# Optimization experiments

Measured on AMD Instinct MI355X. Metric: run time of the kernel, lower is better.

Reference implementation:

```python
import jax, jax.numpy as jnp
import numpy as np

N = 50000          # nodes
E_RAND = 800000    # random edges (avg degree 16)
IN, HID, HEADS, OUT = 256, 64, 4, 40
NEG_SLOPE = 0.2    # PyG GATConv default leaky_relu slope
BN_EPS = 1e-5


def setup_inputs() -> dict:
    key = jax.random.key(0)
    ks = jax.random.split(key, 24)
    x = jax.random.normal(ks[0], (N, IN), jnp.float32)
    ei = jax.random.randint(ks[1], (2, E_RAND), 0, N)
    loops = jnp.arange(N, dtype=ei.dtype)
    edge_index = jnp.concatenate([ei, jnp.stack([loops, loops])], axis=1)  # add self loops (PyG default)
    s = 0.1
    d = {
        "x": x,
        "edge_index": edge_index,
        "W0": jax.random.normal(ks[2], (IN, HEADS * HID), jnp.float32) * s,
        "a_src0": jax.random.normal(ks[3], (HEADS, HID), jnp.float32) * s,
        "a_dst0": jax.random.normal(ks[4], (HEADS, HID), jnp.float32) * s,
        "b0": jax.random.normal(ks[5], (HEADS * HID,), jnp.float32) * s,
        "bn0_g": jnp.ones((HEADS * HID,), jnp.float32),
        "bn0_b": jnp.zeros((HEADS * HID,), jnp.float32),
        "bn0_m": jax.random.normal(ks[6], (HEADS * HID,), jnp.float32) * s,
        "bn0_v": jax.random.uniform(ks[7], (HEADS * HID,), jnp.float32, 0.5, 1.5),
        "W1": jax.random.normal(ks[8], (HEADS * HID, HEADS * HID), jnp.float32) * s,
        "a_src1": jax.random.normal(ks[9], (HEADS, HID), jnp.float32) * s,
        "a_dst1": jax.random.normal(ks[10], (HEADS, HID), jnp.float32) * s,
        "b1": jax.random.normal(ks[11], (HEADS * HID,), jnp.float32) * s,
        "bn1_g": jnp.ones((HEADS * HID,), jnp.float32),
        "bn1_b": jnp.zeros((HEADS * HID,), jnp.float32),
        "bn1_m": jax.random.normal(ks[12], (HEADS * HID,), jnp.float32) * s,
        "bn1_v": jax.random.uniform(ks[13], (HEADS * HID,), jnp.float32, 0.5, 1.5),
        "W2": jax.random.normal(ks[14], (HEADS * HID, OUT), jnp.float32) * s,
        "a_src2": jax.random.normal(ks[15], (1, OUT), jnp.float32) * s,
        "a_dst2": jax.random.normal(ks[16], (1, OUT), jnp.float32) * s,
        "b2": jax.random.normal(ks[17], (OUT,), jnp.float32) * s,
    }
    return d


def gat_conv(x, edge_index, W, att_src, att_dst, heads, ch):
    """PyG GATConv (eval mode): gather -> leaky_relu attn -> segment softmax -> scatter add."""
    src, dst = edge_index[0], edge_index[1]
    h = (x @ W).reshape(-1, heads, ch)                       # [N,H,C]
    a_s = jnp.einsum('nhc,hc->nh', h, att_src)
    a_d = jnp.einsum('nhc,hc->nh', h, att_dst)
    e = jax.nn.leaky_relu(a_s[src] + a_d[dst], NEG_SLOPE)    # [E,H]
    m = jax.ops.segment_max(e, dst, num_segments=N)
    m = jax.lax.stop_gradient(jnp.where(jnp.isfinite(m), m, 0.0))
    p = jnp.exp(e - m[dst])
    denom = jax.ops.segment_sum(p, dst, num_segments=N)
    alpha = p / (denom[dst] + 1e-16)                         # [E,H]
    msg = h[src] * alpha[:, :, None]                         # [E,H,C]
    return jax.ops.segment_sum(msg, dst, num_segments=N)     # [N,H,C]


def _bn(h, g, b, m, v):
    return g * (h - m) * jax.lax.rsqrt(v + BN_EPS) + b


def reference(x, edge_index, W0, a_src0, a_dst0, b0, bn0_g, bn0_b, bn0_m, bn0_v,
              W1, a_src1, a_dst1, b1, bn1_g, bn1_b, bn1_m, bn1_v,
              W2, a_src2, a_dst2, b2):
    h = gat_conv(x, edge_index, W0, a_src0, a_dst0, HEADS, HID).reshape(N, HEADS * HID) + b0
    h = jax.nn.elu(_bn(h, bn0_g, bn0_b, bn0_m, bn0_v))
    h = gat_conv(h, edge_index, W1, a_src1, a_dst1, HEADS, HID).reshape(N, HEADS * HID) + b1
    h = jax.nn.elu(_bn(h, bn1_g, bn1_b, bn1_m, bn1_v))
    out = gat_conv(h, edge_index, W2, a_src2, a_dst2, 1, OUT).reshape(N, OUT) + b2
    return out
```

## Files before the change

kernel.cpp:

```cpp
#include <hip/hip_runtime.h>
#include <cstdint>
#include <cstddef>

constexpr int kN = 50000;
constexpr float kSlope = 0.2f;
constexpr float kBnEps = 1e-5f;

static inline int ceil_div(int a, int b) { return (a + b - 1) / b; }

typedef __attribute__((ext_vector_type(8))) _Float16 half8;
typedef __attribute__((ext_vector_type(8))) unsigned short ushortx8;
typedef __attribute__((ext_vector_type(4))) float f32x4;

__device__ inline unsigned short f2h_us(float f) {
  _Float16 h = (_Float16)f;
  return *(unsigned short*)&h;
}


__global__ void k_degree(const int* __restrict__ dst, int* __restrict__ deg, int E) {
  int e = blockIdx.x * blockDim.x + threadIdx.x;
  if (e < E) atomicAdd(&deg[dst[e]], 1);
}

__global__ void k_scan1(const int* __restrict__ deg, int* __restrict__ rp,
                        int* __restrict__ bsum, int n) {
  __shared__ int sm[256];
  int i = blockIdx.x * 256 + threadIdx.x;
  int v = (i < n) ? deg[i] : 0;
  sm[threadIdx.x] = v;
  __syncthreads();
  for (int off = 1; off < 256; off <<= 1) {
    int t = (threadIdx.x >= off) ? sm[threadIdx.x - off] : 0;
    __syncthreads();
    sm[threadIdx.x] += t;
    __syncthreads();
  }
  if (i < n) rp[i + 1] = sm[threadIdx.x];
  if (threadIdx.x == 255) bsum[blockIdx.x] = sm[255];
}

__global__ void k_scan2(int* bsum, int nb) {
  __shared__ int sm[256];
  int v = (threadIdx.x < nb) ? bsum[threadIdx.x] : 0;
  sm[threadIdx.x] = v;
  __syncthreads();
  for (int off = 1; off < 256; off <<= 1) {
    int t = (threadIdx.x >= off) ? sm[threadIdx.x - off] : 0;
    __syncthreads();
    sm[threadIdx.x] += t;
    __syncthreads();
  }
  if (threadIdx.x < nb) bsum[threadIdx.x] = sm[threadIdx.x] - v;
}

__global__ void k_scan3(int* __restrict__ rp, const int* __restrict__ bsum, int n) {
  int i = blockIdx.x * 256 + threadIdx.x;
  if (i < n) rp[i + 1] += bsum[blockIdx.x];
  if (i == 0) rp[0] = 0;
}

__global__ void k_scatter(const int* __restrict__ src, const int* __restrict__ dst,
                          const int* __restrict__ rp, int* __restrict__ cur,
                          int* __restrict__ csr, int E) {
  int e = blockIdx.x * blockDim.x + threadIdx.x;
  if (e < E) {
    int d = dst[e];
    int pos = rp[d] + atomicAdd(&cur[d], 1);
    csr[pos] = src[e];
  }
}


__global__ void k_cast(const float* __restrict__ in, unsigned short* __restrict__ out, int n4) {
  int i = blockIdx.x * blockDim.x + threadIdx.x;
  if (i >= n4) return;
  float4 v = ((const float4*)in)[i];
  ushort4 o;
  o.x = f2h_us(v.x);
  o.y = f2h_us(v.y);
  o.z = f2h_us(v.z);
  o.w = f2h_us(v.w);
  ((ushort4*)out)[i] = o;
}

__global__ void k_transW3(const float* __restrict__ W0, unsigned short* __restrict__ Wt0,
                          const float* __restrict__ W1, unsigned short* __restrict__ Wt1,
                          const float* __restrict__ W2, unsigned short* __restrict__ Wt2) {
  int i = blockIdx.x * blockDim.x + threadIdx.x;
  const int S0 = 256 * 256, S1 = 256 * 256, S2 = 128 * 256;
  if (i < S0) {
    int nc = i >> 8, k = i & 255;
    Wt0[i] = f2h_us(W0[(size_t)k * 256 + nc]);
  } else if (i < S0 + S1) {
    int j = i - S0;
    int nc = j >> 8, k = j & 255;
    Wt1[j] = f2h_us(W1[(size_t)k * 256 + nc]);
  } else if (i < S0 + S1 + S2) {
    int j = i - S0 - S1;
    int nc = j >> 8, k = j & 255;
    Wt2[j] = (nc < 40) ? f2h_us(W2[(size_t)k * 40 + nc]) : (unsigned short)0;
  }
}


__global__ __launch_bounds__(256) void k_mfma_gemm(
    const unsigned short* __restrict__ A, const unsigned short* __restrict__ Bt,
    unsigned short* __restrict__ C, const float* __restrict__ asrc,
    const float* __restrict__ adst, float* __restrict__ a_s, float* __restrict__ a_d, int M,
    int K, int Nc, int ldc, int heads, int acols) {
  constexpr int BM = 128, BK = 32, LDR = 40;
  __shared__ unsigned short As[BM * LDR];
  __shared__ unsigned short Bs[BM * LDR];
  int tid = threadIdx.x;
  int wave = tid >> 6, lane = tid & 63;
  int quad = lane >> 4, l16 = lane & 15;
  int wm = (wave & 1) * 64, wn = (wave >> 1) * 64;
  int bm = blockIdx.x * BM, bn = blockIdx.y * BM;
  f32x4 acc[4][4] = {};
  for (int k0 = 0; k0 < K; k0 += BK) {
#pragma unroll
    for (int it = 0; it < 2; it++) {
      int c = tid + it * 256;
      int row = c >> 2, part = c & 3;
      int gm = bm + row;
      ushortx8 va = (ushortx8)(0);
      if (gm < M) va = *(const ushortx8*)(A + (size_t)gm * K + k0 + part * 8);
      *(ushortx8*)(As + row * LDR + part * 8) = va;
      ushortx8 vb = *(const ushortx8*)(Bt + (size_t)(bn + row) * K + k0 + part * 8);
      *(ushortx8*)(Bs + row * LDR + part * 8) = vb;
    }
    __syncthreads();
    half8 af[4], bf[4];
#pragma unroll
    for (int i = 0; i < 4; i++) {
      af[i] = *(const half8*)(As + (wm + i * 16 + l16) * LDR + quad * 8);
      bf[i] = *(const half8*)(Bs + (wn + i * 16 + l16) * LDR + quad * 8);
    }
#pragma unroll
    for (int i = 0; i < 4; i++)
#pragma unroll
      for (int j = 0; j < 4; j++)
        acc[i][j] = __builtin_amdgcn_mfma_f32_16x16x32_f16(af[i], bf[j], acc[i][j], 0, 0, 0);
    __syncthreads();
  }
#pragma unroll
  for (int i = 0; i < 4; i++) {
#pragma unroll
    for (int j = 0; j < 4; j++) {
      int col = bn + wn + j * 16 + l16;
      if (col >= Nc) continue;
#pragma unroll
      for (int r = 0; r < 4; r++) {
        int row = bm + wm + i * 16 + quad * 4 + r;
        if (row < M) C[(size_t)row * ldc + col] = f2h_us(acc[i][j][r]);
      }
    }
  }
  int ghead = (bn + wn) >> 6;
  if (ghead < heads) {
    float asv[4], adv[4];
#pragma unroll
    for (int j = 0; j < 4; j++) {
      int col = bn + wn + j * 16 + l16;
      bool ok = col < acols;
      asv[j] = ok ? asrc[col] : 0.f;
      adv[j] = ok ? adst[col] : 0.f;
    }
#pragma unroll
    for (int i = 0; i < 4; i++) {
#pragma unroll
      for (int r = 0; r < 4; r++) {
        float s = acc[i][0][r] * asv[0] + acc[i][1][r] * asv[1] + acc[i][2][r] * asv[2] +
                  acc[i][3][r] * asv[3];
        float d = acc[i][0][r] * adv[0] + acc[i][1][r] * adv[1] + acc[i][2][r] * adv[2] +
                  acc[i][3][r] * adv[3];
#pragma unroll
        for (int mask = 1; mask <= 8; mask <<= 1) {
          s += __shfl_xor(s, mask, 64);
          d += __shfl_xor(d, mask, 64);
        }
        if (l16 == 0) {
          int row = bm + wm + i * 16 + quad * 4 + r;
          if (row < M) {
            a_s[row * heads + ghead] = s;
            a_d[row * heads + ghead] = d;
          }
        }
      }
    }
  }
}


__global__ __launch_bounds__(256) void k_attn_agg256(
    const int* __restrict__ rp, const int* __restrict__ csr, const _Float16* __restrict__ h,
    const float* __restrict__ a_s, const float* __restrict__ a_d, const float* __restrict__ bias,
    const float* __restrict__ bg, const float* __restrict__ bb, const float* __restrict__ bm,
    const float* __restrict__ bv, unsigned short* __restrict__ out, int n_nodes) {
  int wid = (blockIdx.x * blockDim.x + threadIdx.x) >> 6;
  int lane = threadIdx.x & 63;
  if (wid >= n_nodes) return;
  int n = wid;
  int beg = rp[n], end = rp[n + 1];
  int half = lane >> 5, l32 = lane & 31;
  int head = l32 >> 3;
  int c = l32 * 8;
  float ad = a_d[n * 4 + head];
  float acc[8] = {};
  float psum = 0.f;
  int e = beg;
  for (; e + 8 <= end; e += 8) {
    int s0 = csr[e + half];
    int s1 = csr[e + 2 + half];
    int s2 = csr[e + 4 + half];
    int s3 = csr[e + 6 + half];
    float x0 = a_s[s0 * 4 + head] + ad;
    float x1 = a_s[s1 * 4 + head] + ad;
    float x2 = a_s[s2 * 4 + head] + ad;
    float x3 = a_s[s3 * 4 + head] + ad;
    half8 v0 = *(const half8*)(h + (size_t)s0 * 256 + c);
    half8 v1 = *(const half8*)(h + (size_t)s1 * 256 + c);
    half8 v2 = *(const half8*)(h + (size_t)s2 * 256 + c);
    half8 v3 = *(const half8*)(h + (size_t)s3 * 256 + c);
    x0 = x0 > 0.f ? x0 : x0 * kSlope;
    x1 = x1 > 0.f ? x1 : x1 * kSlope;
    x2 = x2 > 0.f ? x2 : x2 * kSlope;
    x3 = x3 > 0.f ? x3 : x3 * kSlope;
    float p0 = __expf(x0), p1 = __expf(x1);
    float p2 = __expf(x2), p3 = __expf(x3);
    psum += (p0 + p1) + (p2 + p3);
#pragma unroll
    for (int j = 0; j < 8; j++) {
      acc[j] += (float)v0[j] * p0 + (float)v1[j] * p1;
      acc[j] += (float)v2[j] * p2 + (float)v3[j] * p3;
    }
  }
  for (; e + 2 <= end; e += 2) {
    int s0 = csr[e + half];
    float x0 = a_s[s0 * 4 + head] + ad;
    x0 = x0 > 0.f ? x0 : x0 * kSlope;
    float p0 = __expf(x0);
    psum += p0;
    half8 v0 = *(const half8*)(h + (size_t)s0 * 256 + c);
#pragma unroll
    for (int j = 0; j < 8; j++) acc[j] += (float)v0[j] * p0;
  }
  if (e < end && half == 0) {
    int s0 = csr[e];
    float x0 = a_s[s0 * 4 + head] + ad;
    x0 = x0 > 0.f ? x0 : x0 * kSlope;
    float p0 = __expf(x0);
    psum += p0;
    half8 v0 = *(const half8*)(h + (size_t)s0 * 256 + c);
#pragma unroll
    for (int j = 0; j < 8; j++) acc[j] += (float)v0[j] * p0;
  }
  psum += __shfl_xor(psum, 32, 64);
#pragma unroll
  for (int j = 0; j < 8; j++) acc[j] += __shfl_xor(acc[j], 32, 64);
  if (half == 0) {
    float rden = 1.f / (psum + 1e-16f);
    ushortx8 o;
#pragma unroll
    for (int j = 0; j < 8; j++) {
      float v = acc[j] * rden + bias[c + j];
      v = bg[c + j] * (v - bm[c + j]) * rsqrtf(bv[c + j] + kBnEps) + bb[c + j];
      v = v > 0.f ? v : (__expf(v) - 1.f);
      o[j] = f2h_us(v);
    }
    *(ushortx8*)(out + (size_t)n * 256 + c) = o;
  }
}


__global__ __launch_bounds__(256) void k_attn_agg40(
    const int* __restrict__ rp, const int* __restrict__ csr, const _Float16* __restrict__ h,
    const float* __restrict__ a_s, const float* __restrict__ a_d, const float* __restrict__ bias,
    float* __restrict__ out, int n_nodes) {
  int wid = (blockIdx.x * blockDim.x + threadIdx.x) >> 6;
  int lane = threadIdx.x & 63;
  if (wid >= n_nodes) return;
  int n = wid;
  int beg = rp[n], end = rp[n + 1];
  float ad = a_d[n];
  int grp = lane >> 3, l8 = lane & 7;
  int c = l8 * 8;
  float acc[8] = {};
  float psum = 0.f;
  for (int base = beg; base < end; base += 16) {
    int e0 = base + grp;
    int e1 = base + 8 + grp;
    if (e0 < end) {
      int s = csr[e0];
      float x = a_s[s] + ad;
      x = x > 0.f ? x : x * kSlope;
      float p = __expf(x);
      psum += p;
      half8 hv = *(const half8*)(h + (size_t)s * 64 + c);
#pragma unroll
      for (int j = 0; j < 8; j++) acc[j] += (float)hv[j] * p;
    }
    if (e1 < end) {
      int s = csr[e1];
      float x = a_s[s] + ad;
      x = x > 0.f ? x : x * kSlope;
      float p = __expf(x);
      psum += p;
      half8 hv = *(const half8*)(h + (size_t)s * 64 + c);
#pragma unroll
      for (int j = 0; j < 8; j++) acc[j] += (float)hv[j] * p;
    }
  }
#pragma unroll
  for (int mask = 8; mask <= 32; mask <<= 1) psum += __shfl_xor(psum, mask, 64);
#pragma unroll
  for (int j = 0; j < 8; j++) {
#pragma unroll
    for (int mask = 8; mask <= 32; mask <<= 1) acc[j] += __shfl_xor(acc[j], mask, 64);
  }
  if (lane < 5) {
    float rden = 1.f / (psum + 1e-16f);
    float4 o0, o1;
    o0.x = acc[0] * rden + bias[c + 0];
    o0.y = acc[1] * rden + bias[c + 1];
    o0.z = acc[2] * rden + bias[c + 2];
    o0.w = acc[3] * rden + bias[c + 3];
    o1.x = acc[4] * rden + bias[c + 4];
    o1.y = acc[5] * rden + bias[c + 5];
    o1.z = acc[6] * rden + bias[c + 6];
    o1.w = acc[7] * rden + bias[c + 7];
    *(float4*)(out + (size_t)n * 40 + c) = o0;
    *(float4*)(out + (size_t)n * 40 + c + 4) = o1;
  }
}


extern "C" void kernel_launch(void* const* d_in, const int* in_sizes, int n_in, void* d_out,
                              int out_size, void* d_ws, size_t ws_size, hipStream_t stream) {
  const float* x = (const float*)d_in[0];
  const int* ei = (const int*)d_in[1];
  const float* W0 = (const float*)d_in[2];
  const float* as0 = (const float*)d_in[3];
  const float* ad0 = (const float*)d_in[4];
  const float* b0 = (const float*)d_in[5];
  const float* bg0 = (const float*)d_in[6];
  const float* bb0 = (const float*)d_in[7];
  const float* bm0 = (const float*)d_in[8];
  const float* bv0 = (const float*)d_in[9];
  const float* W1 = (const float*)d_in[10];
  const float* as1 = (const float*)d_in[11];
  const float* ad1 = (const float*)d_in[12];
  const float* b1 = (const float*)d_in[13];
  const float* bg1 = (const float*)d_in[14];
  const float* bb1 = (const float*)d_in[15];
  const float* bm1 = (const float*)d_in[16];
  const float* bv1 = (const float*)d_in[17];
  const float* W2 = (const float*)d_in[18];
  const float* as2 = (const float*)d_in[19];
  const float* ad2 = (const float*)d_in[20];
  const float* b2 = (const float*)d_in[21];
  float* out = (float*)d_out;

  const int E = in_sizes[1] / 2;
  const int* srcIdx = ei;
  const int* dstIdx = ei + E;

  char* p = (char*)d_ws;
  auto alloc = [&](size_t bytes) -> void* {
    void* r = (void*)p;
    p += (bytes + 255) & ~(size_t)255;
    return r;
  };
  int* rp = (int*)alloc((kN + 1) * sizeof(int));
  int* degcur = (int*)alloc((size_t)2 * kN * sizeof(int));
  int* deg = degcur;
  int* cur = degcur + kN;
  int* bsum = (int*)alloc(256 * sizeof(int));
  int* csr = (int*)alloc((size_t)E * sizeof(int));
  float* a_s = (float*)alloc((size_t)kN * 4 * sizeof(float));
  float* a_d = (float*)alloc((size_t)kN * 4 * sizeof(float));
  unsigned short* x16 = (unsigned short*)alloc((size_t)kN * 256 * 2);
  unsigned short* h16 = (unsigned short*)alloc((size_t)kN * 256 * 2);
  unsigned short* act16 = (unsigned short*)alloc((size_t)kN * 256 * 2);
  unsigned short* Wt0 = (unsigned short*)alloc((size_t)256 * 256 * 2);
  unsigned short* Wt1 = (unsigned short*)alloc((size_t)256 * 256 * 2);
  unsigned short* Wt2 = (unsigned short*)alloc((size_t)128 * 256 * 2);

  const int eb = ceil_div(E, 256);
  const int nb = ceil_div(kN, 256);

  hipMemsetAsync(degcur, 0, (size_t)2 * kN * sizeof(int), stream);
  k_degree<<<eb, 256, 0, stream>>>(dstIdx, deg, E);
  k_scan1<<<nb, 256, 0, stream>>>(deg, rp, bsum, kN);
  k_scan2<<<1, 256, 0, stream>>>(bsum, nb);
  k_scan3<<<nb, 256, 0, stream>>>(rp, bsum, kN);
  k_scatter<<<eb, 256, 0, stream>>>(srcIdx, dstIdx, rp, cur, csr, E);

  k_cast<<<ceil_div(kN * 64, 256), 256, 0, stream>>>(x, x16, kN * 64);
  k_transW3<<<ceil_div(256 * 256 * 2 + 128 * 256, 256), 256, 0, stream>>>(W0, Wt0, W1, Wt1, W2,
                                                                          Wt2);

  dim3 gg(ceil_div(kN, 128), 2);
  dim3 gg2(ceil_div(kN, 128), 1);
  int wpn_blocks = ceil_div(kN, 4);

  k_mfma_gemm<<<gg, 256, 0, stream>>>(x16, Wt0, h16, as0, ad0, a_s, a_d, kN, 256, 256, 256, 4,
                                      256);
  k_attn_agg256<<<wpn_blocks, 256, 0, stream>>>(rp, csr, (const _Float16*)h16, a_s, a_d, b0, bg0,
                                                bb0, bm0, bv0, act16, kN);

  k_mfma_gemm<<<gg, 256, 0, stream>>>(act16, Wt1, h16, as1, ad1, a_s, a_d, kN, 256, 256, 256, 4,
                                      256);
  k_attn_agg256<<<wpn_blocks, 256, 0, stream>>>(rp, csr, (const _Float16*)h16, a_s, a_d, b1, bg1,
                                                bb1, bm1, bv1, act16, kN);

  k_mfma_gemm<<<gg2, 256, 0, stream>>>(act16, Wt2, h16, as2, ad2, a_s, a_d, kN, 256, 40, 64, 1,
                                       40);
  k_attn_agg40<<<wpn_blocks, 256, 0, stream>>>(rp, csr, (const _Float16*)h16, a_s, a_d, b2, out,
                                               kN);
}
```

Before: 462.2 us.

## Use direct global-to-LDS loads in GEMM, widen attention unroll, fuse prep kernels

The GEMM tile staging now uses global_load_lds 16-byte direct loads into unpadded LDS instead of loading through registers and storing to padded shared memory. The attention aggregation kernel gains a 16-edge unrolled loop with eight independent gathers per lane and a launch-bounds occupancy hint. The fp16 cast and weight-transpose kernels are merged into one launch. Dropping the LDS padding may add bank conflicts, and removing the row bound check lets the last GEMM tile read past the end of the activation buffers.

```diff
diff --git a/kernel.cpp b/kernel.cpp
--- a/kernel.cpp
+++ b/kernel.cpp
@@ -15,6 +15,11 @@
 __device__ inline unsigned short f2h_us(float f) {
   _Float16 h = (_Float16)f;
   return *(unsigned short*)&h;
+}
+
+__device__ inline void gload16(const void* g, void* l) {
+  __builtin_amdgcn_global_load_lds((const __attribute__((address_space(1))) unsigned int*)g,
+                                   (__attribute__((address_space(3))) unsigned int*)l, 16, 0, 0);
 }
 
 
@@ -72,34 +77,35 @@
 }
 
 
-__global__ void k_cast(const float* __restrict__ in, unsigned short* __restrict__ out, int n4) {
+__global__ void k_prep(const float* __restrict__ x, unsigned short* __restrict__ x16,
+                       const float* __restrict__ W0, unsigned short* __restrict__ Wt0,
+                       const float* __restrict__ W1, unsigned short* __restrict__ Wt1,
+                       const float* __restrict__ W2, unsigned short* __restrict__ Wt2) {
   int i = blockIdx.x * blockDim.x + threadIdx.x;
-  if (i >= n4) return;
-  float4 v = ((const float4*)in)[i];
-  ushort4 o;
-  o.x = f2h_us(v.x);
-  o.y = f2h_us(v.y);
-  o.z = f2h_us(v.z);
-  o.w = f2h_us(v.w);
-  ((ushort4*)out)[i] = o;
-}
-
-__global__ void k_transW3(const float* __restrict__ W0, unsigned short* __restrict__ Wt0,
-                          const float* __restrict__ W1, unsigned short* __restrict__ Wt1,
-                          const float* __restrict__ W2, unsigned short* __restrict__ Wt2) {
-  int i = blockIdx.x * blockDim.x + threadIdx.x;
+  const int N4 = kN * 64;
   const int S0 = 256 * 256, S1 = 256 * 256, S2 = 128 * 256;
-  if (i < S0) {
-    int nc = i >> 8, k = i & 255;
-    Wt0[i] = f2h_us(W0[(size_t)k * 256 + nc]);
-  } else if (i < S0 + S1) {
-    int j = i - S0;
-    int nc = j >> 8, k = j & 255;
-    Wt1[j] = f2h_us(W1[(size_t)k * 256 + nc]);
-  } else if (i < S0 + S1 + S2) {
-    int j = i - S0 - S1;
-    int nc = j >> 8, k = j & 255;
-    Wt2[j] = (nc < 40) ? f2h_us(W2[(size_t)k * 40 + nc]) : (unsigned short)0;
+  if (i < N4) {
+    float4 v = ((const float4*)x)[i];
+    ushort4 o;
+    o.x = f2h_us(v.x);
+    o.y = f2h_us(v.y);
+    o.z = f2h_us(v.z);
+    o.w = f2h_us(v.w);
+    ((ushort4*)x16)[i] = o;
+  } else {
+    int j = i - N4;
+    if (j < S0) {
+      int nc = j >> 8, k = j & 255;
+      Wt0[j] = f2h_us(W0[(size_t)k * 256 + nc]);
+    } else if (j < S0 + S1) {
+      int t = j - S0;
+      int nc = t >> 8, k = t & 255;
+      Wt1[t] = f2h_us(W1[(size_t)k * 256 + nc]);
+    } else if (j < S0 + S1 + S2) {
+      int t = j - S0 - S1;
+      int nc = t >> 8, k = t & 255;
+      Wt2[t] = (nc < 40) ? f2h_us(W2[(size_t)k * 40 + nc]) : (unsigned short)0;
+    }
   }
 }
 
@@ -109,33 +115,31 @@
     unsigned short* __restrict__ C, const float* __restrict__ asrc,
     const float* __restrict__ adst, float* __restrict__ a_s, float* __restrict__ a_d, int M,
     int K, int Nc, int ldc, int heads, int acols) {
-  constexpr int BM = 128, BK = 32, LDR = 40;
-  __shared__ unsigned short As[BM * LDR];
-  __shared__ unsigned short Bs[BM * LDR];
+  constexpr int BM = 128, BK = 32;
+  __shared__ unsigned short As[BM * BK];
+  __shared__ unsigned short Bs[BM * BK];
   int tid = threadIdx.x;
   int wave = tid >> 6, lane = tid & 63;
   int quad = lane >> 4, l16 = lane & 15;
   int wm = (wave & 1) * 64, wn = (wave >> 1) * 64;
   int bm = blockIdx.x * BM, bn = blockIdx.y * BM;
+  int srow = lane >> 2;
+  int spart = lane & 3;
   f32x4 acc[4][4] = {};
   for (int k0 = 0; k0 < K; k0 += BK) {
 #pragma unroll
     for (int it = 0; it < 2; it++) {
-      int c = tid + it * 256;
-      int row = c >> 2, part = c & 3;
-      int gm = bm + row;
-      ushortx8 va = (ushortx8)(0);
-      if (gm < M) va = *(const ushortx8*)(A + (size_t)gm * K + k0 + part * 8);
-      *(ushortx8*)(As + row * LDR + part * 8) = va;
-      ushortx8 vb = *(const ushortx8*)(Bt + (size_t)(bn + row) * K + k0 + part * 8);
-      *(ushortx8*)(Bs + row * LDR + part * 8) = vb;
+      int chunk = wave * 2 + it;
+      int row = chunk * 16 + srow;
+      gload16(A + (size_t)(bm + row) * K + k0 + spart * 8, As + chunk * 512);
+      gload16(Bt + (size_t)(bn + row) * K + k0 + spart * 8, Bs + chunk * 512);
     }
     __syncthreads();
     half8 af[4], bf[4];
 #pragma unroll
     for (int i = 0; i < 4; i++) {
-      af[i] = *(const half8*)(As + (wm + i * 16 + l16) * LDR + quad * 8);
-      bf[i] = *(const half8*)(Bs + (wn + i * 16 + l16) * LDR + quad * 8);
+      af[i] = *(const half8*)(As + (wm + i * 16 + l16) * BK + quad * 8);
+      bf[i] = *(const half8*)(Bs + (wn + i * 16 + l16) * BK + quad * 8);
     }
 #pragma unroll
     for (int i = 0; i < 4; i++)
@@ -193,7 +197,7 @@
 }
 
 
-__global__ __launch_bounds__(256) void k_attn_agg256(
+__global__ __launch_bounds__(256, 8) void k_attn_agg256(
     const int* __restrict__ rp, const int* __restrict__ csr, const _Float16* __restrict__ h,
     const float* __restrict__ a_s, const float* __restrict__ a_d, const float* __restrict__ bias,
     const float* __restrict__ bg, const float* __restrict__ bb, const float* __restrict__ bm,
@@ -210,6 +214,53 @@
   float acc[8] = {};
   float psum = 0.f;
   int e = beg;
+  for (; e + 16 <= end; e += 16) {
+    int eb = e + half * 8;
+    int s0 = csr[eb + 0];
+    int s1 = csr[eb + 1];
+    int s2 = csr[eb + 2];
+    int s3 = csr[eb + 3];
+    int s4 = csr[eb + 4];
+    int s5 = csr[eb + 5];
+    int s6 = csr[eb + 6];
+    int s7 = csr[eb + 7];
+    float t0 = a_s[s0 * 4 + head];
+    float t1 = a_s[s1 * 4 + head];
+    float t2 = a_s[s2 * 4 + head];
+    float t3 = a_s[s3 * 4 + head];
+    float t4 = a_s[s4 * 4 + head];
+    float t5 = a_s[s5 * 4 + head];
+    float t6 = a_s[s6 * 4 + head];
+    float t7 = a_s[s7 * 4 + head];
+    half8 v0 = *(const half8*)(h + (size_t)s0 * 256 + c);
+    half8 v1 = *(const half8*)(h + (size_t)s1 * 256 + c);
+    half8 v2 = *(const half8*)(h + (size_t)s2 * 256 + c);
+    half8 v3 = *(const half8*)(h + (size_t)s3 * 256 + c);
+    half8 v4 = *(const half8*)(h + (size_t)s4 * 256 + c);
+    half8 v5 = *(const half8*)(h + (size_t)s5 * 256 + c);
+    half8 v6 = *(const half8*)(h + (size_t)s6 * 256 + c);
+    half8 v7 = *(const half8*)(h + (size_t)s7 * 256 + c);
+    float x0 = t0 + ad, x1 = t1 + ad, x2 = t2 + ad, x3 = t3 + ad;
+    float x4 = t4 + ad, x5 = t5 + ad, x6 = t6 + ad, x7 = t7 + ad;
+    x0 = x0 > 0.f ? x0 : x0 * kSlope;
+    x1 = x1 > 0.f ? x1 : x1 * kSlope;
+    x2 = x2 > 0.f ? x2 : x2 * kSlope;
+    x3 = x3 > 0.f ? x3 : x3 * kSlope;
+    x4 = x4 > 0.f ? x4 : x4 * kSlope;
+    x5 = x5 > 0.f ? x5 : x5 * kSlope;
+    x6 = x6 > 0.f ? x6 : x6 * kSlope;
+    x7 = x7 > 0.f ? x7 : x7 * kSlope;
+    float p0 = __expf(x0), p1 = __expf(x1), p2 = __expf(x2), p3 = __expf(x3);
+    float p4 = __expf(x4), p5 = __expf(x5), p6 = __expf(x6), p7 = __expf(x7);
+    psum += ((p0 + p1) + (p2 + p3)) + ((p4 + p5) + (p6 + p7));
+#pragma unroll
+    for (int j = 0; j < 8; j++) {
+      acc[j] += (float)v0[j] * p0 + (float)v1[j] * p1;
+      acc[j] += (float)v2[j] * p2 + (float)v3[j] * p3;
+      acc[j] += (float)v4[j] * p4 + (float)v5[j] * p5;
+      acc[j] += (float)v6[j] * p6 + (float)v7[j] * p7;
+    }
+  }
   for (; e + 8 <= end; e += 8) {
     int s0 = csr[e + half];
     int s1 = csr[e + 2 + half];
@@ -397,9 +448,8 @@
   k_scan3<<<nb, 256, 0, stream>>>(rp, bsum, kN);
   k_scatter<<<eb, 256, 0, stream>>>(srcIdx, dstIdx, rp, cur, csr, E);
 
-  k_cast<<<ceil_div(kN * 64, 256), 256, 0, stream>>>(x, x16, kN * 64);
-  k_transW3<<<ceil_div(256 * 256 * 2 + 128 * 256, 256), 256, 0, stream>>>(W0, Wt0, W1, Wt1, W2,
-                                                                          Wt2);
+  const int prep_items = kN * 64 + 256 * 256 * 2 + 128 * 256;
+  k_prep<<<ceil_div(prep_items, 256), 256, 0, stream>>>(x, x16, W0, Wt0, W1, Wt1, W2, Wt2);
 
   dim3 gg(ceil_div(kN, 128), 2);
   dim3 gg2(ceil_div(kN, 128), 1);
```

Result: slower. 474.0 us (+2.6%).
